# Optimization experiments

Hardware: AMD Instinct MI355X
Metric: run time of the kernel (lower is better)

The kernel has to match this reference:

```python
import jax, jax.numpy as jnp
import numpy as np

N, C, A = 1024, 200, 256
P, Q, EPS = 0.8, 2.0, 0.01  # cls_Loss defaults


def setup_inputs() -> dict:
    key = jax.random.key(0)
    ks = jax.random.split(key, 7)
    return {
        "fc_weight": jax.random.normal(ks[0], (C, A), jnp.float32) * 0.05,
        "features_source": jax.random.normal(ks[1], (N, A), jnp.float32),
        "y_s": jax.random.normal(ks[2], (N, C), jnp.float32),
        "labels_source": jax.random.randint(ks[3], (N,), 0, C),
        "Lambda": jnp.float32(0.5),
        "mean_source": jax.random.normal(ks[4], (C, A), jnp.float32),
        "mean_target": jax.random.normal(ks[5], (C, A), jnp.float32),
        "covariance_target": jax.random.normal(ks[6], (C, A, A), jnp.float32) * 0.01,
    }


def _aug(fc_weight, y_s, labels, Lambda, mean_s, mean_t, cov_t):
    # D[n,c,:] = W[c] - W[labels[n]]   (NxW_ij - NxW_kj)
    D = fc_weight[None, :, :] - fc_weight[labels][:, None, :]  # [N,C,A]
    CVn = cov_t[labels]                                        # [N,A,A]
    # diagonal of D @ CV @ D^T computed directly (no NxCxC intermediate)
    M = jnp.einsum('nab,ncb->nca', CVn, D)                     # [N,C,A]
    sigma2 = Lambda * jnp.sum(D * M, axis=-1)                  # [N,C]
    dmean = mean_t[labels] - mean_s[labels]                    # [N,A]
    shift = jnp.einsum('nca,na->nc', D, dmean)                 # [N,C]
    return y_s + 0.5 * sigma2 + Lambda * shift


def _cls_loss(outputs, targets):
    n = outputs.shape[0]
    # accumulated starts at zero buffer -> equals per-class counts of this batch
    counts = jnp.zeros((C,), jnp.float32).at[targets].add(1.0)
    acc = jnp.maximum(counts, 1.0)
    matrix = acc[None, :] / acc[:, None]                       # [C,C]
    sample_w = jnp.where(matrix < 1.0, matrix ** P, 1.0)
    mitigation = sample_w[targets]                             # [N,C]
    scores = jax.nn.softmax(jax.lax.stop_gradient(outputs), axis=1)
    self_scores = scores[jnp.arange(n), targets]               # [N]
    score_matrix = scores / jnp.maximum(self_scores, EPS)[:, None]
    compensation = jnp.where(score_matrix > 1.0, score_matrix ** Q, 1.0)
    seesaw = mitigation * compensation                         # [N,C]
    onehot = jax.nn.one_hot(targets, C, dtype=outputs.dtype)
    logits = outputs + jnp.log(seesaw) * (1.0 - onehot)
    logp = jax.nn.log_softmax(logits, axis=1)
    nll = -jnp.take_along_axis(logp, targets[:, None], axis=1)[:, 0]
    return jnp.mean(nll)


def reference(fc_weight, features_source, y_s, labels_source, Lambda,
              mean_source, mean_target, covariance_target):
    # features_source only provides N, A in the original; not used numerically
    aug_y = _aug(fc_weight, y_s, labels_source, Lambda,
                 mean_source, mean_target, covariance_target)
    return _cls_loss(aug_y, labels_source)
```

## Files before the change

kernel.cpp:

```cpp
#include <hip/hip_runtime.h>
#include <hip/hip_fp16.h>
#include <math.h>

#define NN 1024
#define CC 200
#define AA 256

static constexpr float P_EXP = 0.8f;
static constexpr float Q_EXP = 2.0f;
static constexpr float EPS_C = 0.01f;

typedef __attribute__((ext_vector_type(8))) _Float16 half8;
typedef __attribute__((ext_vector_type(4))) _Float16 half4v;
typedef __attribute__((ext_vector_type(4))) float f32x4;

__global__ void k_prep(const float* __restrict__ W, const int* __restrict__ lab,
                       _Float16* __restrict__ Whf, float* __restrict__ accv){
  if (blockIdx.x == 52){
    __shared__ int cnt[CC];
    int t = threadIdx.x;
    for (int i = t; i < CC; i += 256) cnt[i] = 0;
    __syncthreads();
    for (int n = t; n < NN; n += 256) atomicAdd(&cnt[lab[n]], 1);
    __syncthreads();
    for (int i = t; i < CC; i += 256) accv[i] = fmaxf((float)cnt[i], 1.0f);
    return;
  }
  int idx = (blockIdx.x * 256 + threadIdx.x) * 4;
  if (idx >= 208 * AA) return;
  float4 w = make_float4(0.f, 0.f, 0.f, 0.f);
  if (idx < CC * AA) w = *(const float4*)(W + idx);
  Whf[idx + 0] = (_Float16)w.x;
  Whf[idx + 1] = (_Float16)w.y;
  Whf[idx + 2] = (_Float16)w.z;
  Whf[idx + 3] = (_Float16)w.w;
}

__global__ __launch_bounds__(512) void k_quad(
    const _Float16* __restrict__ Whf, const float* __restrict__ CV,
    const float* __restrict__ ms, const float* __restrict__ mtg,
    const float* __restrict__ lamp, float* __restrict__ tbl)
{
  const int l    = blockIdx.x;
  const int tid  = threadIdx.x;
  const int wid  = tid >> 6;
  const int lane = tid & 63;
  const int lrow = lane & 15;
  const int kgrp = lane >> 4;

  __shared__ float4 cvb[2][16][64];
  __shared__ _Float16 dmh[AA];

  if (tid < AA)
    dmh[tid] = (_Float16)(2.f * (mtg[l * AA + tid] - ms[l * AA + tid]));

  const int ct0 = wid, ct1 = wid + 8;
  half8 ef0[8], ef1[8];
  #pragma unroll
  for (int kt = 0; kt < 8; ++kt){
    half8 wlv = *(const half8*)(Whf + l * AA + kt * 32 + kgrp * 8);
    half8 wc0 = *(const half8*)(Whf + (ct0 * 16 + lrow) * AA + kt * 32 + kgrp * 8);
    ef0[kt] = wc0 - wlv;
    if (wid < 5){
      half8 wc1 = *(const half8*)(Whf + (ct1 * 16 + lrow) * AA + kt * 32 + kgrp * 8);
      ef1[kt] = wc1 - wlv;
    }
  }

  const size_t cvbase = (size_t)l * AA * AA;

  #define STAGE(TILE, BUF) do {                                               \
    int r0_ = wid * 2;                                                        \
    _Pragma("unroll")                                                         \
    for (int rr_ = 0; rr_ < 2; ++rr_){                                        \
      int row_ = r0_ + rr_;                                                   \
      const float* gs_ = CV + cvbase + (size_t)(TILE) * 16 * AA               \
                       + (size_t)row_ * AA + ((lane ^ (row_ & 7)) << 2);      \
      __builtin_amdgcn_global_load_lds(                                       \
        (const __attribute__((address_space(1))) void*)gs_,                   \
        (__attribute__((address_space(3))) void*)&cvb[BUF][row_][0],          \
        16, 0, 0);                                                            \
    }                                                                         \
  } while(0)

  STAGE(0, 0);
  __syncthreads();

  f32x4 D2a = {0.f,0.f,0.f,0.f}, D2b = {0.f,0.f,0.f,0.f};
  const float lam = lamp[0];

  for (int t = 0; t < 16; ++t){
    if (t + 1 < 16) STAGE(t + 1, (t + 1) & 1);

    const int buf = t & 1;
    f32x4 a0 = {0.f,0.f,0.f,0.f}, a1 = {0.f,0.f,0.f,0.f};
    #pragma unroll
    for (int kt = 0; kt < 8; ++kt){
      const int j0 = kt * 8 + kgrp * 2;
      float4 v0 = cvb[buf][lrow][( j0     ) ^ (lrow & 7)];
      float4 v1 = cvb[buf][lrow][( j0 + 1 ) ^ (lrow & 7)];
      half8 cvf;
      cvf[0]=(_Float16)v0.x; cvf[1]=(_Float16)v0.y; cvf[2]=(_Float16)v0.z; cvf[3]=(_Float16)v0.w;
      cvf[4]=(_Float16)v1.x; cvf[5]=(_Float16)v1.y; cvf[6]=(_Float16)v1.z; cvf[7]=(_Float16)v1.w;
      a0 = __builtin_amdgcn_mfma_f32_16x16x32_f16(cvf, ef0[kt], a0, 0, 0, 0);
      if (wid < 5)
        a1 = __builtin_amdgcn_mfma_f32_16x16x32_f16(cvf, ef1[kt], a1, 0, 0, 0);
    }

    half4v dmf = *(const half4v*)&dmh[t * 16 + kgrp * 4];
    half4v wl2 = *(const half4v*)(Whf + l * AA + t * 16 + kgrp * 4);
    {
      half4v wc2 = *(const half4v*)(Whf + (ct0 * 16 + lrow) * AA + t * 16 + kgrp * 4);
      half4v e2  = wc2 - wl2;
      half4v b2;
      b2[0]=(_Float16)a0[0]; b2[1]=(_Float16)a0[1]; b2[2]=(_Float16)a0[2]; b2[3]=(_Float16)a0[3];
      D2a = __builtin_amdgcn_mfma_f32_16x16x16f16(e2, b2,  D2a, 0, 0, 0);
      D2a = __builtin_amdgcn_mfma_f32_16x16x16f16(e2, dmf, D2a, 0, 0, 0);
    }
    if (wid < 5){
      half4v wc2 = *(const half4v*)(Whf + (ct1 * 16 + lrow) * AA + t * 16 + kgrp * 4);
      half4v e2  = wc2 - wl2;
      half4v b2;
      b2[0]=(_Float16)a1[0]; b2[1]=(_Float16)a1[1]; b2[2]=(_Float16)a1[2]; b2[3]=(_Float16)a1[3];
      D2b = __builtin_amdgcn_mfma_f32_16x16x16f16(e2, b2,  D2b, 0, 0, 0);
      D2b = __builtin_amdgcn_mfma_f32_16x16x16f16(e2, dmf, D2b, 0, 0, 0);
    }
    __syncthreads();
  }

  if ((lrow >> 2) == kgrp){
    const int jj = lrow & 3;
    const int c0 = ct0 * 16 + lrow;
    float d0 = (jj == 0) ? D2a[0] : (jj == 1) ? D2a[1] : (jj == 2) ? D2a[2] : D2a[3];
    if (c0 < CC) tbl[l * CC + c0] = 0.5f * lam * d0;
    if (wid < 5){
      const int c1 = ct1 * 16 + lrow;
      float d1 = (jj == 0) ? D2b[0] : (jj == 1) ? D2b[1] : (jj == 2) ? D2b[2] : D2b[3];
      if (c1 < CC) tbl[l * CC + c1] = 0.5f * lam * d1;
    }
  }
  #undef STAGE
}

__global__ __launch_bounds__(64) void k_rows(
    const float* __restrict__ ys, const int* __restrict__ lab,
    const float* __restrict__ accv, const float* __restrict__ tbl,
    float* __restrict__ nll)
{
  const int n    = blockIdx.x;
  const int lane = threadIdx.x;
  const int l    = lab[n];
  const float acc_l = accv[l];
  const float log_acc_l = logf(acc_l);

  float z[4];
  float m = -1e30f;
  #pragma unroll
  for (int k = 0; k < 4; k++){
    int cidx = k * 64 + lane;
    float zz = (cidx < CC) ? (ys[n * CC + cidx] + tbl[l * CC + cidx]) : -1e30f;
    z[k] = zz;
    m = fmaxf(m, zz);
  }
  for (int o = 32; o; o >>= 1) m = fmaxf(m, __shfl_xor(m, o));

  float se = 0.f;
  #pragma unroll
  for (int k = 0; k < 4; k++){
    int cidx = k * 64 + lane;
    if (cidx < CC) se += expf(z[k] - m);
  }
  for (int o = 32; o; o >>= 1) se += __shfl_xor(se, o);
  const float L0 = m + logf(se);

  const int kl = l >> 6, ll = l & 63;
  float zsel = (kl == 0) ? z[0] : (kl == 1 ? z[1] : (kl == 2 ? z[2] : z[3]));
  const float zl = __shfl(zsel, ll);
  const float logden = fmaxf(zl - L0, logf(EPS_C));

  float lg[4];
  float m2 = -1e30f;
  #pragma unroll
  for (int k = 0; k < 4; k++){
    int cidx = k * 64 + lane;
    float lz = -1e30f;
    if (cidx < CC){
      lz = z[k];
      if (cidx != l){
        float lratio = (z[k] - L0) - logden;
        float lcomp  = (lratio > 0.f) ? Q_EXP * lratio : 0.f;
        float accc   = accv[cidx];
        float lmit   = (accc < acc_l) ? P_EXP * (logf(accc) - log_acc_l) : 0.f;
        lz += lcomp + lmit;
      }
    }
    lg[k] = lz;
    m2 = fmaxf(m2, lz);
  }
  for (int o = 32; o; o >>= 1) m2 = fmaxf(m2, __shfl_xor(m2, o));
  float se2 = 0.f;
  #pragma unroll
  for (int k = 0; k < 4; k++){
    int cidx = k * 64 + lane;
    if (cidx < CC) se2 += expf(lg[k] - m2);
  }
  for (int o = 32; o; o >>= 1) se2 += __shfl_xor(se2, o);
  const float L1 = m2 + logf(se2);

  if (lane == 0) nll[n] = L1 - zl;
}

__global__ void k_mean(const float* __restrict__ nll, float* __restrict__ out){
  __shared__ float s[256];
  int t = threadIdx.x;
  float v = 0.f;
  for (int i = t; i < NN; i += 256) v += nll[i];
  s[t] = v; __syncthreads();
  for (int o = 128; o; o >>= 1){ if (t < o) s[t] += s[t + o]; __syncthreads(); }
  if (t == 0) out[0] = s[0] / (float)NN;
}

extern "C" void kernel_launch(void* const* d_in, const int* in_sizes, int n_in,
                              void* d_out, int out_size, void* d_ws, size_t ws_size,
                              hipStream_t stream) {
  const float* W   = (const float*)d_in[0];
  const float* ys  = (const float*)d_in[2];
  const int*   lab = (const int*)  d_in[3];
  const float* lam = (const float*)d_in[4];
  const float* ms  = (const float*)d_in[5];
  const float* mt  = (const float*)d_in[6];
  const float* CV  = (const float*)d_in[7];

  float* ws   = (float*)d_ws;
  float* tbl  = ws;
  float* accv = ws + 40000;
  float* nll  = ws + 40256;
  _Float16* Whf = (_Float16*)(ws + 41280);
  float* out  = (float*)d_out;

  k_prep <<<53, 256, 0, stream>>>(W, lab, Whf, accv);
  k_quad <<<CC, 512, 0, stream>>>(Whf, CV, ms, mt, lam, tbl);
  k_rows <<<NN, 64, 0, stream>>>(ys, lab, accv, tbl, nll);
  k_mean <<<1, 256, 0, stream>>>(nll, out);
}
```

Measured before the change: 46.16 us.

## Split quad kernel over two A-halves and triple-buffer covariance staging

The covariance quadratic-form kernel now launches a 2×C grid, with each block handling half of the A rows of one class's covariance. The two partial tables go to separate workspace slots and are summed in the row kernel. The staging also moves from double to triple buffering with explicit waitcnt and barriers, so two tiles stay in flight. This roughly doubles block count on a 200-block launch to fill more CUs and hide memory latency, at the cost of an extra table read per row and duplicated W-difference register setup per block.

```diff
diff --git a/kernel.cpp b/kernel.cpp
--- a/kernel.cpp
+++ b/kernel.cpp
@@ -41,18 +41,19 @@
     const float* __restrict__ ms, const float* __restrict__ mtg,
     const float* __restrict__ lamp, float* __restrict__ tbl)
 {
-  const int l    = blockIdx.x;
+  const int ah   = blockIdx.x;
+  const int l    = blockIdx.y;
   const int tid  = threadIdx.x;
   const int wid  = tid >> 6;
   const int lane = tid & 63;
   const int lrow = lane & 15;
   const int kgrp = lane >> 4;
 
-  __shared__ float4 cvb[2][16][64];
-  __shared__ _Float16 dmh[AA];
-
-  if (tid < AA)
-    dmh[tid] = (_Float16)(2.f * (mtg[l * AA + tid] - ms[l * AA + tid]));
+  __shared__ float4 cvb[3][16][64];
+  __shared__ _Float16 dmh[128];
+
+  if (tid < 128)
+    dmh[tid] = (_Float16)(2.f * (mtg[l * AA + ah * 128 + tid] - ms[l * AA + ah * 128 + tid]));
 
   const int ct0 = wid, ct1 = wid + 8;
   half8 ef0[8], ef1[8];
@@ -67,13 +68,12 @@
     }
   }
 
-  const size_t cvbase = (size_t)l * AA * AA;
+  const size_t cvbase = (size_t)l * AA * AA + (size_t)ah * 128 * AA;
 
   #define STAGE(TILE, BUF) do {                                               \
-    int r0_ = wid * 2;                                                        \
     _Pragma("unroll")                                                         \
     for (int rr_ = 0; rr_ < 2; ++rr_){                                        \
-      int row_ = r0_ + rr_;                                                   \
+      int row_ = wid * 2 + rr_;                                               \
       const float* gs_ = CV + cvbase + (size_t)(TILE) * 16 * AA               \
                        + (size_t)row_ * AA + ((lane ^ (row_ & 7)) << 2);      \
       __builtin_amdgcn_global_load_lds(                                       \
@@ -84,15 +84,25 @@
   } while(0)
 
   STAGE(0, 0);
-  __syncthreads();
+  STAGE(1, 1);
+  asm volatile("s_waitcnt vmcnt(2) lgkmcnt(0)" ::: "memory");
+  __builtin_amdgcn_sched_barrier(0);
+  __builtin_amdgcn_s_barrier();
+  __builtin_amdgcn_sched_barrier(0);
 
   f32x4 D2a = {0.f,0.f,0.f,0.f}, D2b = {0.f,0.f,0.f,0.f};
   const float lam = lamp[0];
 
-  for (int t = 0; t < 16; ++t){
-    if (t + 1 < 16) STAGE(t + 1, (t + 1) & 1);
-
-    const int buf = t & 1;
+  for (int t = 0; t < 8; ++t){
+    const int aslg = ah * 128 + t * 16 + kgrp * 4;
+    half4v wl2 = *(const half4v*)(Whf + l * AA + aslg);
+    half4v wc2a = *(const half4v*)(Whf + (ct0 * 16 + lrow) * AA + aslg);
+    half4v wc2b = wl2;
+    if (wid < 5) wc2b = *(const half4v*)(Whf + (ct1 * 16 + lrow) * AA + aslg);
+
+    if (t + 2 < 8) STAGE(t + 2, (t + 2) % 3);
+
+    const int buf = t % 3;
     f32x4 a0 = {0.f,0.f,0.f,0.f}, a1 = {0.f,0.f,0.f,0.f};
     #pragma unroll
     for (int kt = 0; kt < 8; ++kt){
@@ -108,35 +118,36 @@
     }
 
     half4v dmf = *(const half4v*)&dmh[t * 16 + kgrp * 4];
-    half4v wl2 = *(const half4v*)(Whf + l * AA + t * 16 + kgrp * 4);
     {
-      half4v wc2 = *(const half4v*)(Whf + (ct0 * 16 + lrow) * AA + t * 16 + kgrp * 4);
-      half4v e2  = wc2 - wl2;
+      half4v e2 = wc2a - wl2;
       half4v b2;
       b2[0]=(_Float16)a0[0]; b2[1]=(_Float16)a0[1]; b2[2]=(_Float16)a0[2]; b2[3]=(_Float16)a0[3];
       D2a = __builtin_amdgcn_mfma_f32_16x16x16f16(e2, b2,  D2a, 0, 0, 0);
       D2a = __builtin_amdgcn_mfma_f32_16x16x16f16(e2, dmf, D2a, 0, 0, 0);
     }
     if (wid < 5){
-      half4v wc2 = *(const half4v*)(Whf + (ct1 * 16 + lrow) * AA + t * 16 + kgrp * 4);
-      half4v e2  = wc2 - wl2;
+      half4v e2 = wc2b - wl2;
       half4v b2;
       b2[0]=(_Float16)a1[0]; b2[1]=(_Float16)a1[1]; b2[2]=(_Float16)a1[2]; b2[3]=(_Float16)a1[3];
       D2b = __builtin_amdgcn_mfma_f32_16x16x16f16(e2, b2,  D2b, 0, 0, 0);
       D2b = __builtin_amdgcn_mfma_f32_16x16x16f16(e2, dmf, D2b, 0, 0, 0);
     }
-    __syncthreads();
+
+    asm volatile("s_waitcnt vmcnt(2) lgkmcnt(0)" ::: "memory");
+    __builtin_amdgcn_sched_barrier(0);
+    __builtin_amdgcn_s_barrier();
+    __builtin_amdgcn_sched_barrier(0);
   }
 
   if ((lrow >> 2) == kgrp){
     const int jj = lrow & 3;
     const int c0 = ct0 * 16 + lrow;
     float d0 = (jj == 0) ? D2a[0] : (jj == 1) ? D2a[1] : (jj == 2) ? D2a[2] : D2a[3];
-    if (c0 < CC) tbl[l * CC + c0] = 0.5f * lam * d0;
+    if (c0 < CC) tbl[(size_t)ah * CC * CC + l * CC + c0] = 0.5f * lam * d0;
     if (wid < 5){
       const int c1 = ct1 * 16 + lrow;
       float d1 = (jj == 0) ? D2b[0] : (jj == 1) ? D2b[1] : (jj == 2) ? D2b[2] : D2b[3];
-      if (c1 < CC) tbl[l * CC + c1] = 0.5f * lam * d1;
+      if (c1 < CC) tbl[(size_t)ah * CC * CC + l * CC + c1] = 0.5f * lam * d1;
     }
   }
   #undef STAGE
@@ -158,7 +169,9 @@
   #pragma unroll
   for (int k = 0; k < 4; k++){
     int cidx = k * 64 + lane;
-    float zz = (cidx < CC) ? (ys[n * CC + cidx] + tbl[l * CC + cidx]) : -1e30f;
+    float zz = -1e30f;
+    if (cidx < CC)
+      zz = ys[n * CC + cidx] + tbl[l * CC + cidx] + tbl[CC * CC + l * CC + cidx];
     z[k] = zz;
     m = fmaxf(m, zz);
   }
@@ -233,13 +246,14 @@
 
   float* ws   = (float*)d_ws;
   float* tbl  = ws;
-  float* accv = ws + 40000;
-  float* nll  = ws + 40256;
-  _Float16* Whf = (_Float16*)(ws + 41280);
+  float* accv = ws + 80000;
+  float* nll  = ws + 80256;
+  _Float16* Whf = (_Float16*)(ws + 81280);
   float* out  = (float*)d_out;
 
   k_prep <<<53, 256, 0, stream>>>(W, lab, Whf, accv);
-  k_quad <<<CC, 512, 0, stream>>>(Whf, CV, ms, mt, lam, tbl);
+  dim3 gq(2, CC);
+  k_quad <<<gq, 512, 0, stream>>>(Whf, CV, ms, mt, lam, tbl);
   k_rows <<<NN, 64, 0, stream>>>(ys, lab, accv, tbl, nll);
   k_mean <<<1, 256, 0, stream>>>(nll, out);
 }
```

Measured after the change: 50.20 us. 8.7% more time.

## Split quadratic-form kernel across 4 row-chunks of covariance per label

Applied to the files above, without the earlier changes.

k_quad now runs a 4xC grid of 256-thread blocks. Each block handles 64 rows of one label's covariance matrix and writes a partial table, and k_rows sums the four partials. The aim is to give 800 blocks instead of 200 so more CUs stream the covariance data in parallel. In exchange, W-difference fragments are reloaded inside the loop rather than held in registers, tbl grows fourfold, and k_rows does extra reads.

```diff
diff --git a/kernel.cpp b/kernel.cpp
--- a/kernel.cpp
+++ b/kernel.cpp
@@ -36,12 +36,13 @@
   Whf[idx + 3] = (_Float16)w.w;
 }
 
-__global__ __launch_bounds__(512) void k_quad(
+__global__ __launch_bounds__(256) void k_quad(
     const _Float16* __restrict__ Whf, const float* __restrict__ CV,
     const float* __restrict__ ms, const float* __restrict__ mtg,
     const float* __restrict__ lamp, float* __restrict__ tbl)
 {
-  const int l    = blockIdx.x;
+  const int q    = blockIdx.x;
+  const int l    = blockIdx.y;
   const int tid  = threadIdx.x;
   const int wid  = tid >> 6;
   const int lane = tid & 63;
@@ -49,31 +50,17 @@
   const int kgrp = lane >> 4;
 
   __shared__ float4 cvb[2][16][64];
-  __shared__ _Float16 dmh[AA];
-
-  if (tid < AA)
-    dmh[tid] = (_Float16)(2.f * (mtg[l * AA + tid] - ms[l * AA + tid]));
-
-  const int ct0 = wid, ct1 = wid + 8;
-  half8 ef0[8], ef1[8];
-  #pragma unroll
-  for (int kt = 0; kt < 8; ++kt){
-    half8 wlv = *(const half8*)(Whf + l * AA + kt * 32 + kgrp * 8);
-    half8 wc0 = *(const half8*)(Whf + (ct0 * 16 + lrow) * AA + kt * 32 + kgrp * 8);
-    ef0[kt] = wc0 - wlv;
-    if (wid < 5){
-      half8 wc1 = *(const half8*)(Whf + (ct1 * 16 + lrow) * AA + kt * 32 + kgrp * 8);
-      ef1[kt] = wc1 - wlv;
-    }
-  }
-
-  const size_t cvbase = (size_t)l * AA * AA;
+  __shared__ _Float16 dmh[64];
+
+  if (tid < 64)
+    dmh[tid] = (_Float16)(2.f * (mtg[l * AA + q * 64 + tid] - ms[l * AA + q * 64 + tid]));
+
+  const size_t cvbase = (size_t)l * AA * AA + (size_t)q * 64 * AA;
 
   #define STAGE(TILE, BUF) do {                                               \
-    int r0_ = wid * 2;                                                        \
     _Pragma("unroll")                                                         \
-    for (int rr_ = 0; rr_ < 2; ++rr_){                                        \
-      int row_ = r0_ + rr_;                                                   \
+    for (int rr_ = 0; rr_ < 4; ++rr_){                                        \
+      int row_ = wid * 4 + rr_;                                               \
       const float* gs_ = CV + cvbase + (size_t)(TILE) * 16 * AA               \
                        + (size_t)row_ * AA + ((lane ^ (row_ & 7)) << 2);      \
       __builtin_amdgcn_global_load_lds(                                       \
@@ -86,14 +73,19 @@
   STAGE(0, 0);
   __syncthreads();
 
-  f32x4 D2a = {0.f,0.f,0.f,0.f}, D2b = {0.f,0.f,0.f,0.f};
+  f32x4 D2[4];
+  #pragma unroll
+  for (int k = 0; k < 4; ++k) D2[k] = (f32x4){0.f,0.f,0.f,0.f};
   const float lam = lamp[0];
 
-  for (int t = 0; t < 16; ++t){
-    if (t + 1 < 16) STAGE(t + 1, (t + 1) & 1);
+  for (int t = 0; t < 4; ++t){
+    if (t + 1 < 4) STAGE(t + 1, (t + 1) & 1);
 
     const int buf = t & 1;
-    f32x4 a0 = {0.f,0.f,0.f,0.f}, a1 = {0.f,0.f,0.f,0.f};
+    f32x4 a[4];
+    #pragma unroll
+    for (int k = 0; k < 4; ++k) a[k] = (f32x4){0.f,0.f,0.f,0.f};
+
     #pragma unroll
     for (int kt = 0; kt < 8; ++kt){
       const int j0 = kt * 8 + kgrp * 2;
@@ -102,41 +94,48 @@
       half8 cvf;
       cvf[0]=(_Float16)v0.x; cvf[1]=(_Float16)v0.y; cvf[2]=(_Float16)v0.z; cvf[3]=(_Float16)v0.w;
       cvf[4]=(_Float16)v1.x; cvf[5]=(_Float16)v1.y; cvf[6]=(_Float16)v1.z; cvf[7]=(_Float16)v1.w;
-      a0 = __builtin_amdgcn_mfma_f32_16x16x32_f16(cvf, ef0[kt], a0, 0, 0, 0);
-      if (wid < 5)
-        a1 = __builtin_amdgcn_mfma_f32_16x16x32_f16(cvf, ef1[kt], a1, 0, 0, 0);
-    }
-
+      half8 wlv = *(const half8*)(Whf + l * AA + kt * 32 + kgrp * 8);
+      #pragma unroll
+      for (int k = 0; k < 4; ++k){
+        const int ct = wid + k * 4;
+        if (ct < 13){
+          half8 wcf = *(const half8*)(Whf + (ct * 16 + lrow) * AA + kt * 32 + kgrp * 8);
+          a[k] = __builtin_amdgcn_mfma_f32_16x16x32_f16(cvf, wcf - wlv, a[k], 0, 0, 0);
+        }
+      }
+    }
+
+    const int aslg = q * 64 + t * 16 + kgrp * 4;
+    half4v wl2 = *(const half4v*)(Whf + l * AA + aslg);
     half4v dmf = *(const half4v*)&dmh[t * 16 + kgrp * 4];
-    half4v wl2 = *(const half4v*)(Whf + l * AA + t * 16 + kgrp * 4);
-    {
-      half4v wc2 = *(const half4v*)(Whf + (ct0 * 16 + lrow) * AA + t * 16 + kgrp * 4);
-      half4v e2  = wc2 - wl2;
-      half4v b2;
-      b2[0]=(_Float16)a0[0]; b2[1]=(_Float16)a0[1]; b2[2]=(_Float16)a0[2]; b2[3]=(_Float16)a0[3];
-      D2a = __builtin_amdgcn_mfma_f32_16x16x16f16(e2, b2,  D2a, 0, 0, 0);
-      D2a = __builtin_amdgcn_mfma_f32_16x16x16f16(e2, dmf, D2a, 0, 0, 0);
-    }
-    if (wid < 5){
-      half4v wc2 = *(const half4v*)(Whf + (ct1 * 16 + lrow) * AA + t * 16 + kgrp * 4);
-      half4v e2  = wc2 - wl2;
-      half4v b2;
-      b2[0]=(_Float16)a1[0]; b2[1]=(_Float16)a1[1]; b2[2]=(_Float16)a1[2]; b2[3]=(_Float16)a1[3];
-      D2b = __builtin_amdgcn_mfma_f32_16x16x16f16(e2, b2,  D2b, 0, 0, 0);
-      D2b = __builtin_amdgcn_mfma_f32_16x16x16f16(e2, dmf, D2b, 0, 0, 0);
-    }
+    #pragma unroll
+    for (int k = 0; k < 4; ++k){
+      const int ct = wid + k * 4;
+      if (ct < 13){
+        half4v wc2 = *(const half4v*)(Whf + (ct * 16 + lrow) * AA + aslg);
+        half4v e2  = wc2 - wl2;
+        half4v b2;
+        b2[0]=(_Float16)a[k][0]; b2[1]=(_Float16)a[k][1];
+        b2[2]=(_Float16)a[k][2]; b2[3]=(_Float16)a[k][3];
+        D2[k] = __builtin_amdgcn_mfma_f32_16x16x16f16(e2, b2,  D2[k], 0, 0, 0);
+        D2[k] = __builtin_amdgcn_mfma_f32_16x16x16f16(e2, dmf, D2[k], 0, 0, 0);
+      }
+    }
+
     __syncthreads();
   }
 
   if ((lrow >> 2) == kgrp){
     const int jj = lrow & 3;
-    const int c0 = ct0 * 16 + lrow;
-    float d0 = (jj == 0) ? D2a[0] : (jj == 1) ? D2a[1] : (jj == 2) ? D2a[2] : D2a[3];
-    if (c0 < CC) tbl[l * CC + c0] = 0.5f * lam * d0;
-    if (wid < 5){
-      const int c1 = ct1 * 16 + lrow;
-      float d1 = (jj == 0) ? D2b[0] : (jj == 1) ? D2b[1] : (jj == 2) ? D2b[2] : D2b[3];
-      if (c1 < CC) tbl[l * CC + c1] = 0.5f * lam * d1;
+    #pragma unroll
+    for (int k = 0; k < 4; ++k){
+      const int ct = wid + k * 4;
+      const int c  = ct * 16 + lrow;
+      if (ct < 13 && c < CC){
+        float d = (jj == 0) ? D2[k][0] : (jj == 1) ? D2[k][1]
+                : (jj == 2) ? D2[k][2] : D2[k][3];
+        tbl[(size_t)q * CC * CC + l * CC + c] = 0.5f * lam * d;
+      }
     }
   }
   #undef STAGE
@@ -158,7 +157,12 @@
   #pragma unroll
   for (int k = 0; k < 4; k++){
     int cidx = k * 64 + lane;
-    float zz = (cidx < CC) ? (ys[n * CC + cidx] + tbl[l * CC + cidx]) : -1e30f;
+    float zz = -1e30f;
+    if (cidx < CC){
+      zz = ys[n * CC + cidx]
+         + tbl[             l * CC + cidx] + tbl[    CC * CC + l * CC + cidx]
+         + tbl[2 * CC * CC + l * CC + cidx] + tbl[3 * CC * CC + l * CC + cidx];
+    }
     z[k] = zz;
     m = fmaxf(m, zz);
   }
@@ -233,13 +237,14 @@
 
   float* ws   = (float*)d_ws;
   float* tbl  = ws;
-  float* accv = ws + 40000;
-  float* nll  = ws + 40256;
-  _Float16* Whf = (_Float16*)(ws + 41280);
+  float* accv = ws + 160000;
+  float* nll  = ws + 160256;
+  _Float16* Whf = (_Float16*)(ws + 161280);
   float* out  = (float*)d_out;
 
   k_prep <<<53, 256, 0, stream>>>(W, lab, Whf, accv);
-  k_quad <<<CC, 512, 0, stream>>>(Whf, CV, ms, mt, lam, tbl);
+  dim3 gq(4, CC);
+  k_quad <<<gq, 256, 0, stream>>>(Whf, CV, ms, mt, lam, tbl);
   k_rows <<<NN, 64, 0, stream>>>(ys, lab, accv, tbl, nll);
   k_mean <<<1, 256, 0, stream>>>(nll, out);
 }
```

After: 96.35 us. 2.09x slower.

## Split covariance quadratic form across four row-quarter blocks per label

Applied to the files above, without the earlier changes.

The k_quad grid grows from 200 blocks to 4x200 so each block handles a 64-row quarter of the label's covariance matrix. Each block writes a partial quadratic-form table, and k_rows sums the four partials. This is meant to raise occupancy and memory parallelism on a GPU with many more CUs than 200 blocks could fill. In exchange, the W-difference fragments are recomputed in every block and the partial table is four times larger, which adds extra reads in k_rows.

```diff
diff --git a/kernel.cpp b/kernel.cpp
--- a/kernel.cpp
+++ b/kernel.cpp
@@ -41,7 +41,8 @@
     const float* __restrict__ ms, const float* __restrict__ mtg,
     const float* __restrict__ lamp, float* __restrict__ tbl)
 {
-  const int l    = blockIdx.x;
+  const int q    = blockIdx.x;
+  const int l    = blockIdx.y;
   const int tid  = threadIdx.x;
   const int wid  = tid >> 6;
   const int lane = tid & 63;
@@ -49,10 +50,10 @@
   const int kgrp = lane >> 4;
 
   __shared__ float4 cvb[2][16][64];
-  __shared__ _Float16 dmh[AA];
-
-  if (tid < AA)
-    dmh[tid] = (_Float16)(2.f * (mtg[l * AA + tid] - ms[l * AA + tid]));
+  __shared__ _Float16 dmh[64];
+
+  if (tid < 64)
+    dmh[tid] = (_Float16)(2.f * (mtg[l * AA + q * 64 + tid] - ms[l * AA + q * 64 + tid]));
 
   const int ct0 = wid, ct1 = wid + 8;
   half8 ef0[8], ef1[8];
@@ -67,13 +68,12 @@
     }
   }
 
-  const size_t cvbase = (size_t)l * AA * AA;
+  const size_t cvbase = (size_t)l * AA * AA + (size_t)q * 64 * AA;
 
   #define STAGE(TILE, BUF) do {                                               \
-    int r0_ = wid * 2;                                                        \
     _Pragma("unroll")                                                         \
     for (int rr_ = 0; rr_ < 2; ++rr_){                                        \
-      int row_ = r0_ + rr_;                                                   \
+      int row_ = wid * 2 + rr_;                                               \
       const float* gs_ = CV + cvbase + (size_t)(TILE) * 16 * AA               \
                        + (size_t)row_ * AA + ((lane ^ (row_ & 7)) << 2);      \
       __builtin_amdgcn_global_load_lds(                                       \
@@ -89,8 +89,8 @@
   f32x4 D2a = {0.f,0.f,0.f,0.f}, D2b = {0.f,0.f,0.f,0.f};
   const float lam = lamp[0];
 
-  for (int t = 0; t < 16; ++t){
-    if (t + 1 < 16) STAGE(t + 1, (t + 1) & 1);
+  for (int t = 0; t < 4; ++t){
+    if (t + 1 < 4) STAGE(t + 1, (t + 1) & 1);
 
     const int buf = t & 1;
     f32x4 a0 = {0.f,0.f,0.f,0.f}, a1 = {0.f,0.f,0.f,0.f};
@@ -107,10 +107,11 @@
         a1 = __builtin_amdgcn_mfma_f32_16x16x32_f16(cvf, ef1[kt], a1, 0, 0, 0);
     }
 
+    const int aslg = q * 64 + t * 16 + kgrp * 4;
+    half4v wl2 = *(const half4v*)(Whf + l * AA + aslg);
     half4v dmf = *(const half4v*)&dmh[t * 16 + kgrp * 4];
-    half4v wl2 = *(const half4v*)(Whf + l * AA + t * 16 + kgrp * 4);
     {
-      half4v wc2 = *(const half4v*)(Whf + (ct0 * 16 + lrow) * AA + t * 16 + kgrp * 4);
+      half4v wc2 = *(const half4v*)(Whf + (ct0 * 16 + lrow) * AA + aslg);
       half4v e2  = wc2 - wl2;
       half4v b2;
       b2[0]=(_Float16)a0[0]; b2[1]=(_Float16)a0[1]; b2[2]=(_Float16)a0[2]; b2[3]=(_Float16)a0[3];
@@ -118,13 +119,14 @@
       D2a = __builtin_amdgcn_mfma_f32_16x16x16f16(e2, dmf, D2a, 0, 0, 0);
     }
     if (wid < 5){
-      half4v wc2 = *(const half4v*)(Whf + (ct1 * 16 + lrow) * AA + t * 16 + kgrp * 4);
+      half4v wc2 = *(const half4v*)(Whf + (ct1 * 16 + lrow) * AA + aslg);
       half4v e2  = wc2 - wl2;
       half4v b2;
       b2[0]=(_Float16)a1[0]; b2[1]=(_Float16)a1[1]; b2[2]=(_Float16)a1[2]; b2[3]=(_Float16)a1[3];
       D2b = __builtin_amdgcn_mfma_f32_16x16x16f16(e2, b2,  D2b, 0, 0, 0);
       D2b = __builtin_amdgcn_mfma_f32_16x16x16f16(e2, dmf, D2b, 0, 0, 0);
     }
+
     __syncthreads();
   }
 
@@ -132,11 +134,11 @@
     const int jj = lrow & 3;
     const int c0 = ct0 * 16 + lrow;
     float d0 = (jj == 0) ? D2a[0] : (jj == 1) ? D2a[1] : (jj == 2) ? D2a[2] : D2a[3];
-    if (c0 < CC) tbl[l * CC + c0] = 0.5f * lam * d0;
+    if (c0 < CC) tbl[(size_t)q * CC * CC + l * CC + c0] = 0.5f * lam * d0;
     if (wid < 5){
       const int c1 = ct1 * 16 + lrow;
       float d1 = (jj == 0) ? D2b[0] : (jj == 1) ? D2b[1] : (jj == 2) ? D2b[2] : D2b[3];
-      if (c1 < CC) tbl[l * CC + c1] = 0.5f * lam * d1;
+      if (c1 < CC) tbl[(size_t)q * CC * CC + l * CC + c1] = 0.5f * lam * d1;
     }
   }
   #undef STAGE
@@ -158,7 +160,12 @@
   #pragma unroll
   for (int k = 0; k < 4; k++){
     int cidx = k * 64 + lane;
-    float zz = (cidx < CC) ? (ys[n * CC + cidx] + tbl[l * CC + cidx]) : -1e30f;
+    float zz = -1e30f;
+    if (cidx < CC){
+      zz = ys[n * CC + cidx]
+         + tbl[              l * CC + cidx] + tbl[    CC * CC + l * CC + cidx]
+         + tbl[2 * CC * CC + l * CC + cidx] + tbl[3 * CC * CC + l * CC + cidx];
+    }
     z[k] = zz;
     m = fmaxf(m, zz);
   }
@@ -233,13 +240,14 @@
 
   float* ws   = (float*)d_ws;
   float* tbl  = ws;
-  float* accv = ws + 40000;
-  float* nll  = ws + 40256;
-  _Float16* Whf = (_Float16*)(ws + 41280);
+  float* accv = ws + 160000;
+  float* nll  = ws + 160256;
+  _Float16* Whf = (_Float16*)(ws + 161280);
   float* out  = (float*)d_out;
 
   k_prep <<<53, 256, 0, stream>>>(W, lab, Whf, accv);
-  k_quad <<<CC, 512, 0, stream>>>(Whf, CV, ms, mt, lam, tbl);
+  dim3 gq(4, CC);
+  k_quad <<<gq, 512, 0, stream>>>(Whf, CV, ms, mt, lam, tbl);
   k_rows <<<NN, 64, 0, stream>>>(ys, lab, accv, tbl, nll);
   k_mean <<<1, 256, 0, stream>>>(nll, out);
 }
```

After: 56.81 us. 23.1% more time.
